# Kernel optimization log

Hardware: AMD Instinct MI355X
Metric: run time of the kernel (lower is better)

The kernel has to match this reference:

```python
import jax, jax.numpy as jnp
import numpy as np

IN_C, H, W = 64, 256, 256
K = 3
OUT_C = 128


def setup_inputs() -> dict:
    key = jax.random.key(0)
    k1, k2 = jax.random.split(key)
    x = jax.random.normal(k1, (IN_C, H, W), dtype=jnp.float32)
    limit = np.sqrt(6.0 / (IN_C * K * K + OUT_C)).astype(np.float32)
    kernels = jax.random.uniform(k2, (OUT_C, IN_C, K, K), minval=-limit, maxval=limit, dtype=jnp.float32)
    biases = jnp.zeros((OUT_C,), dtype=jnp.float32)
    return {"x": x, "kernels": kernels, "biases": biases}


def reference(x, kernels, biases):
    # Cross-correlation (patch * kernel, no flip), VALID padding, CHW single image.
    out = jax.lax.conv_general_dilated(
        x[None],                      # [1, C, H, W]
        kernels,                      # [O, I, K, K]
        window_strides=(1, 1),
        padding="VALID",
        dimension_numbers=("NCHW", "OIHW", "NCHW"),
    )[0]                              # [O, H-K+1, W-K+1]
    return out + biases[:, None, None]
```

## Files before the change

kernel.cpp:

```cpp
#include <hip/hip_runtime.h>
#include <stdint.h>

#define IN_C 64
#define HH 256
#define WW 256
#define HW (HH * WW)
#define OUT_C 128
#define OH 254
#define OW 254
#define OHW (OH * OW)

#define XR 4
#define XW 66
#define CPAD 72

typedef __attribute__((ext_vector_type(4))) float f32x4;
typedef __attribute__((ext_vector_type(8))) __bf16 bf16x8;

__device__ __forceinline__ unsigned short f2bf(float f) {
  union { float f; unsigned u; } v; v.f = f;
  unsigned r = v.u + 0x7FFFu + ((v.u >> 16) & 1u);
  return (unsigned short)(r >> 16);
}

__global__ void prep_w(const float* __restrict__ w, unsigned short* __restrict__ wt) {
  const int idx = blockIdx.x * 256 + threadIdx.x;
  if (idx >= 9 * 8192) return;
  const int j    = idx & 7;
  const int lane = (idx >> 3) & 63;
  const int mt   = (idx >> 9) & 7;
  const int ch   = (idx >> 12) & 1;
  const int tap  = idx >> 13;
  const int o = mt * 16 + (lane & 15);
  const int c = ch * 32 + (lane >> 4) * 8 + j;
  wt[idx] = f2bf(w[(o * IN_C + c) * 9 + tap]);
}

__global__ __launch_bounds__(256, 2) void conv_mfma(
    const float* __restrict__ x, const unsigned short* __restrict__ wt,
    const float* __restrict__ bias, float* __restrict__ out) {
  __shared__ __align__(16) unsigned short Xs[XR * XW * CPAD];

  const int tid  = threadIdx.x;
  const int wave = tid >> 6;
  const int lane = tid & 63;
  const int x0 = blockIdx.x * 64;
  const int y0 = blockIdx.y * 2;

  const int mhalf = wave & 1;
  const int nhalf = wave >> 1;
  const int nlane = lane & 15;
  const int quad  = lane >> 4;

  const bf16x8* __restrict__ Wp = ((const bf16x8*)wt) + lane + (mhalf * 4) * 64;

  bf16x8 afA[4], afB[4];
#pragma unroll
  for (int mt = 0; mt < 4; ++mt) afA[mt] = Wp[mt * 64];

  {
    const int cq = tid & 15;
    const int xh = tid >> 4;
    const float* bx = x + (y0 * WW + x0 + xh * 4);
#pragma unroll
    for (int r = 0; r < XR; ++r) {
      f32x4 vv[4];
#pragma unroll
      for (int cc = 0; cc < 4; ++cc)
        vv[cc] = *(const f32x4*)(bx + (cq * 4 + cc) * HW + r * WW);
#pragma unroll
      for (int xxi = 0; xxi < 4; ++xxi) {
        union { unsigned u[2]; } p;
        p.u[0] = (unsigned)f2bf(vv[0][xxi]) | ((unsigned)f2bf(vv[1][xxi]) << 16);
        p.u[1] = (unsigned)f2bf(vv[2][xxi]) | ((unsigned)f2bf(vv[3][xxi]) << 16);
        *(uint2*)&Xs[(r * XW + xh * 4 + xxi) * CPAD + cq * 4] = make_uint2(p.u[0], p.u[1]);
      }
    }
    if (tid < 128) {
      const int c = tid & 63;
      const int xxt = 64 + (tid >> 6);
      int xg = x0 + xxt;
      if (xg > WW - 1) xg = WW - 1;
#pragma unroll
      for (int r = 0; r < XR; ++r)
        Xs[(r * XW + xxt) * CPAD + c] = f2bf(x[c * HW + (y0 + r) * WW + xg]);
    }
  }

  f32x4 acc[4][4];
#pragma unroll
  for (int mt = 0; mt < 4; ++mt) {
    const f32x4 bv = *(const f32x4*)(bias + (mhalf * 4 + mt) * 16 + quad * 4);
#pragma unroll
    for (int nt = 0; nt < 4; ++nt) acc[mt][nt] = bv;
  }

  __syncthreads();

#pragma unroll 1
  for (int pair = 0; pair < 9; ++pair) {
    const int ky = pair / 3;
    const int kx = pair - ky * 3;
    const int r = nhalf + ky;
    const unsigned short* xrow = &Xs[(r * XW + kx) * CPAD + quad * 8];

#pragma unroll
    for (int mt = 0; mt < 4; ++mt) afB[mt] = Wp[((2 * pair + 1) * 8 + mt) * 64];

    {
      bf16x8 bfr[4];
#pragma unroll
      for (int nt = 0; nt < 4; ++nt)
        bfr[nt] = *(const bf16x8*)&xrow[(nt * 16 + nlane) * CPAD];
#pragma unroll
      for (int mt = 0; mt < 4; ++mt)
#pragma unroll
        for (int nt = 0; nt < 4; ++nt)
          acc[mt][nt] = __builtin_amdgcn_mfma_f32_16x16x32_bf16(afA[mt], bfr[nt], acc[mt][nt], 0, 0, 0);
    }

    if (pair < 8) {
#pragma unroll
      for (int mt = 0; mt < 4; ++mt) afA[mt] = Wp[((2 * pair + 2) * 8 + mt) * 64];
    }

    {
      bf16x8 bfr[4];
#pragma unroll
      for (int nt = 0; nt < 4; ++nt)
        bfr[nt] = *(const bf16x8*)&xrow[(nt * 16 + nlane) * CPAD + 32];
#pragma unroll
      for (int mt = 0; mt < 4; ++mt)
#pragma unroll
        for (int nt = 0; nt < 4; ++nt)
          acc[mt][nt] = __builtin_amdgcn_mfma_f32_16x16x32_bf16(afB[mt], bfr[nt], acc[mt][nt], 0, 0, 0);
    }
  }

  const int y = y0 + nhalf;
#pragma unroll
  for (int mt = 0; mt < 4; ++mt) {
    const int obase = (mhalf * 4 + mt) * 16 + quad * 4;
#pragma unroll
    for (int nt = 0; nt < 4; ++nt) {
      const int xc = x0 + nt * 16 + nlane;
      if (xc < OW) {
        float* dst = out + obase * OHW + y * OW + xc;
#pragma unroll
        for (int reg = 0; reg < 4; ++reg)
          dst[reg * OHW] = acc[mt][nt][reg];
      }
    }
  }
}

extern "C" void kernel_launch(void* const* d_in, const int* in_sizes, int n_in,
                              void* d_out, int out_size, void* d_ws, size_t ws_size,
                              hipStream_t stream) {
  const float* x = (const float*)d_in[0];
  const float* w = (const float*)d_in[1];
  const float* b = (const float*)d_in[2];
  float* out = (float*)d_out;
  unsigned short* wt = (unsigned short*)d_ws;

  prep_w<<<dim3(288), dim3(256), 0, stream>>>(w, wt);
  conv_mfma<<<dim3(4, 127), dim3(256), 0, stream>>>(x, wt, b, out);
}
```

Measured before the change: 89.61 us.

## Pre-convert input to swizzled bf16 HWC layout and stage it via async LDS loads

Adds a prep_x kernel that converts the fp32 CHW input once into a bf16 channel-last layout, storing it in workspace with an XOR swizzle on 16-byte channel chunks. The conv kernel then fills its LDS tile with global_load_lds direct-to-LDS copies, replacing per-block fp32 loads, bf16 conversion and scattered LDS stores. Fragment reads apply the matching XOR swizzle in place of the old padded-row layout to avoid bank conflicts. The cost is an extra launch plus a full read and write pass over the input. The last column block also reads past the row into the next row's or trailing memory; those values feed only outputs that are masked off.

```diff
diff --git a/kernel.cpp b/kernel.cpp
--- a/kernel.cpp
+++ b/kernel.cpp
@@ -10,9 +10,9 @@
 #define OW 254
 #define OHW (OH * OW)
 
-#define XR 4
-#define XW 66
-#define CPAD 72
+#define XB_OFF 262144
+#define XROW 72
+#define XRB (XROW * 128)
 
 typedef __attribute__((ext_vector_type(4))) float f32x4;
 typedef __attribute__((ext_vector_type(8))) __bf16 bf16x8;
@@ -21,6 +21,12 @@
   union { float f; unsigned u; } v; v.f = f;
   unsigned r = v.u + 0x7FFFu + ((v.u >> 16) & 1u);
   return (unsigned short)(r >> 16);
+}
+
+__device__ __forceinline__ void async_lds16(const void* g, void* l) {
+  __builtin_amdgcn_global_load_lds(
+      (const __attribute__((address_space(1))) unsigned int*)g,
+      (__attribute__((address_space(3))) unsigned int*)l, 16, 0, 0);
 }
 
 __global__ void prep_w(const float* __restrict__ w, unsigned short* __restrict__ wt) {
@@ -36,10 +42,37 @@
   wt[idx] = f2bf(w[(o * IN_C + c) * 9 + tap]);
 }
 
+__global__ __launch_bounds__(256) void prep_x(const float* __restrict__ x,
+                                              unsigned short* __restrict__ xb) {
+  const int y = blockIdx.x;
+  const int t = threadIdx.x;
+  const int co = t & 7;
+  const int pg = t >> 3;
+  const float* bx = x + (co * 8) * HW + y * WW + pg * 8;
+  f32x4 v[8][2];
+#pragma unroll
+  for (int cc = 0; cc < 8; ++cc) {
+    v[cc][0] = *(const f32x4*)(bx + cc * HW);
+    v[cc][1] = *(const f32x4*)(bx + cc * HW + 4);
+  }
+#pragma unroll
+  for (int i = 0; i < 8; ++i) {
+    unsigned u[4];
+#pragma unroll
+    for (int p = 0; p < 4; ++p) {
+      const float a = (i < 4) ? v[2 * p][0][i] : v[2 * p][1][i - 4];
+      const float b = (i < 4) ? v[2 * p + 1][0][i] : v[2 * p + 1][1][i - 4];
+      u[p] = (unsigned)f2bf(a) | ((unsigned)f2bf(b) << 16);
+    }
+    const int px = pg * 8 + i;
+    *(uint4*)&xb[(((y * WW + px) * 8) + (co ^ i)) * 8] = make_uint4(u[0], u[1], u[2], u[3]);
+  }
+}
+
 __global__ __launch_bounds__(256, 2) void conv_mfma(
-    const float* __restrict__ x, const unsigned short* __restrict__ wt,
+    const unsigned short* __restrict__ xb, const unsigned short* __restrict__ wt,
     const float* __restrict__ bias, float* __restrict__ out) {
-  __shared__ __align__(16) unsigned short Xs[XR * XW * CPAD];
+  __shared__ __align__(16) char Xs[4 * XRB];
 
   const int tid  = threadIdx.x;
   const int wave = tid >> 6;
@@ -53,37 +86,19 @@
   const int quad  = lane >> 4;
 
   const bf16x8* __restrict__ Wp = ((const bf16x8*)wt) + lane + (mhalf * 4) * 64;
-
   bf16x8 afA[4], afB[4];
 #pragma unroll
   for (int mt = 0; mt < 4; ++mt) afA[mt] = Wp[mt * 64];
 
   {
-    const int cq = tid & 15;
-    const int xh = tid >> 4;
-    const float* bx = x + (y0 * WW + x0 + xh * 4);
+    const char* gb = (const char*)xb;
 #pragma unroll
-    for (int r = 0; r < XR; ++r) {
-      f32x4 vv[4];
-#pragma unroll
-      for (int cc = 0; cc < 4; ++cc)
-        vv[cc] = *(const f32x4*)(bx + (cq * 4 + cc) * HW + r * WW);
-#pragma unroll
-      for (int xxi = 0; xxi < 4; ++xxi) {
-        union { unsigned u[2]; } p;
-        p.u[0] = (unsigned)f2bf(vv[0][xxi]) | ((unsigned)f2bf(vv[1][xxi]) << 16);
-        p.u[1] = (unsigned)f2bf(vv[2][xxi]) | ((unsigned)f2bf(vv[3][xxi]) << 16);
-        *(uint2*)&Xs[(r * XW + xh * 4 + xxi) * CPAD + cq * 4] = make_uint2(p.u[0], p.u[1]);
-      }
-    }
-    if (tid < 128) {
-      const int c = tid & 63;
-      const int xxt = 64 + (tid >> 6);
-      int xg = x0 + xxt;
-      if (xg > WW - 1) xg = WW - 1;
-#pragma unroll
-      for (int r = 0; r < XR; ++r)
-        Xs[(r * XW + xxt) * CPAD + c] = f2bf(x[c * HW + (y0 + r) * WW + xg]);
+    for (int i = 0; i < 9; ++i) {
+      const int c = wave + i * 4;
+      const int r = c / 9;
+      const int k = c - r * 9;
+      async_lds16(gb + (size_t)((y0 + r) * WW + x0) * 128 + k * 1024 + lane * 16,
+                  Xs + r * XRB + k * 1024);
     }
   }
 
@@ -102,7 +117,10 @@
     const int ky = pair / 3;
     const int kx = pair - ky * 3;
     const int r = nhalf + ky;
-    const unsigned short* xrow = &Xs[(r * XW + kx) * CPAD + quad * 8];
+    const int sw = (kx + nlane) & 7;
+    const char* xrow = Xs + r * XRB + (kx + nlane) * 128;
+    const int j0 = (quad ^ sw) * 16;
+    const int j1 = ((4 + quad) ^ sw) * 16;
 
 #pragma unroll
     for (int mt = 0; mt < 4; ++mt) afB[mt] = Wp[((2 * pair + 1) * 8 + mt) * 64];
@@ -111,7 +129,7 @@
       bf16x8 bfr[4];
 #pragma unroll
       for (int nt = 0; nt < 4; ++nt)
-        bfr[nt] = *(const bf16x8*)&xrow[(nt * 16 + nlane) * CPAD];
+        bfr[nt] = *(const bf16x8*)(xrow + nt * 2048 + j0);
 #pragma unroll
       for (int mt = 0; mt < 4; ++mt)
 #pragma unroll
@@ -128,7 +146,7 @@
       bf16x8 bfr[4];
 #pragma unroll
       for (int nt = 0; nt < 4; ++nt)
-        bfr[nt] = *(const bf16x8*)&xrow[(nt * 16 + nlane) * CPAD + 32];
+        bfr[nt] = *(const bf16x8*)(xrow + nt * 2048 + j1);
 #pragma unroll
       for (int mt = 0; mt < 4; ++mt)
 #pragma unroll
@@ -162,7 +180,9 @@
   const float* b = (const float*)d_in[2];
   float* out = (float*)d_out;
   unsigned short* wt = (unsigned short*)d_ws;
+  unsigned short* xb = (unsigned short*)((char*)d_ws + XB_OFF);
 
   prep_w<<<dim3(288), dim3(256), 0, stream>>>(w, wt);
-  conv_mfma<<<dim3(4, 127), dim3(256), 0, stream>>>(x, wt, b, out);
+  prep_x<<<dim3(256), dim3(256), 0, stream>>>(x, xb);
+  conv_mfma<<<dim3(4, 127), dim3(256), 0, stream>>>(xb, wt, b, out);
 }
```

Measured after the change: 94.63 us. 1.06x slower.

## Compute four output rows per block with 512 threads to reuse input halo

Applied to the files above, without the earlier changes.

Each block now loads six input rows into LDS and has eight waves compute four output rows, instead of four input rows feeding two output rows with four waves. This lowers the redundant halo loads and fp32-to-bf16 conversions per output row, and halves the grid. It adds row clamping for the final partial tile and bounds checks on stores. The cost is larger LDS per block and fewer, larger blocks, which may reduce occupancy and load balance across CUs.

```diff
diff --git a/kernel.cpp b/kernel.cpp
--- a/kernel.cpp
+++ b/kernel.cpp
@@ -10,7 +10,7 @@
 #define OW 254
 #define OHW (OH * OW)
 
-#define XR 4
+#define XR 6
 #define XW 66
 #define CPAD 72
 
@@ -36,7 +36,7 @@
   wt[idx] = f2bf(w[(o * IN_C + c) * 9 + tap]);
 }
 
-__global__ __launch_bounds__(256, 2) void conv_mfma(
+__global__ __launch_bounds__(512, 2) void conv_mfma(
     const float* __restrict__ x, const unsigned short* __restrict__ wt,
     const float* __restrict__ bias, float* __restrict__ out) {
   __shared__ __align__(16) unsigned short Xs[XR * XW * CPAD];
@@ -45,45 +45,47 @@
   const int wave = tid >> 6;
   const int lane = tid & 63;
   const int x0 = blockIdx.x * 64;
-  const int y0 = blockIdx.y * 2;
+  const int y0 = blockIdx.y * 4;
 
   const int mhalf = wave & 1;
-  const int nhalf = wave >> 1;
+  const int row   = wave >> 1;
   const int nlane = lane & 15;
   const int quad  = lane >> 4;
 
   const bf16x8* __restrict__ Wp = ((const bf16x8*)wt) + lane + (mhalf * 4) * 64;
-
   bf16x8 afA[4], afB[4];
 #pragma unroll
   for (int mt = 0; mt < 4; ++mt) afA[mt] = Wp[mt * 64];
 
   {
     const int cq = tid & 15;
-    const int xh = tid >> 4;
-    const float* bx = x + (y0 * WW + x0 + xh * 4);
+    const int xh = (tid >> 4) & 15;
+    const int r3 = (tid >> 8) * 3;
 #pragma unroll
-    for (int r = 0; r < XR; ++r) {
+    for (int k = 0; k < 3; ++k) {
+      const int r = r3 + k;
+      const int yr = (y0 + r > 255) ? 255 : (y0 + r);
+      const float* bx = x + yr * WW + x0 + xh * 4;
       f32x4 vv[4];
 #pragma unroll
       for (int cc = 0; cc < 4; ++cc)
-        vv[cc] = *(const f32x4*)(bx + (cq * 4 + cc) * HW + r * WW);
+        vv[cc] = *(const f32x4*)(bx + (cq * 4 + cc) * HW);
 #pragma unroll
       for (int xxi = 0; xxi < 4; ++xxi) {
-        union { unsigned u[2]; } p;
-        p.u[0] = (unsigned)f2bf(vv[0][xxi]) | ((unsigned)f2bf(vv[1][xxi]) << 16);
-        p.u[1] = (unsigned)f2bf(vv[2][xxi]) | ((unsigned)f2bf(vv[3][xxi]) << 16);
-        *(uint2*)&Xs[(r * XW + xh * 4 + xxi) * CPAD + cq * 4] = make_uint2(p.u[0], p.u[1]);
+        unsigned u0 = (unsigned)f2bf(vv[0][xxi]) | ((unsigned)f2bf(vv[1][xxi]) << 16);
+        unsigned u1 = (unsigned)f2bf(vv[2][xxi]) | ((unsigned)f2bf(vv[3][xxi]) << 16);
+        *(uint2*)&Xs[(r * XW + xh * 4 + xxi) * CPAD + cq * 4] = make_uint2(u0, u1);
       }
     }
-    if (tid < 128) {
-      const int c = tid & 63;
-      const int xxt = 64 + (tid >> 6);
+    for (int k = tid; k < 768; k += 512) {
+      const int c = k & 63;
+      const int q = k >> 6;
+      const int xxt = 64 + (q & 1);
+      const int r = q >> 1;
+      const int yr = (y0 + r > 255) ? 255 : (y0 + r);
       int xg = x0 + xxt;
       if (xg > WW - 1) xg = WW - 1;
-#pragma unroll
-      for (int r = 0; r < XR; ++r)
-        Xs[(r * XW + xxt) * CPAD + c] = f2bf(x[c * HW + (y0 + r) * WW + xg]);
+      Xs[(r * XW + xxt) * CPAD + c] = f2bf(x[c * HW + yr * WW + xg]);
     }
   }
 
@@ -101,7 +103,7 @@
   for (int pair = 0; pair < 9; ++pair) {
     const int ky = pair / 3;
     const int kx = pair - ky * 3;
-    const int r = nhalf + ky;
+    const int r = row + ky;
     const unsigned short* xrow = &Xs[(r * XW + kx) * CPAD + quad * 8];
 
 #pragma unroll
@@ -137,18 +139,20 @@
     }
   }
 
-  const int y = y0 + nhalf;
+  const int y = y0 + row;
+  if (y < OH) {
 #pragma unroll
-  for (int mt = 0; mt < 4; ++mt) {
-    const int obase = (mhalf * 4 + mt) * 16 + quad * 4;
+    for (int mt = 0; mt < 4; ++mt) {
+      const int obase = (mhalf * 4 + mt) * 16 + quad * 4;
 #pragma unroll
-    for (int nt = 0; nt < 4; ++nt) {
-      const int xc = x0 + nt * 16 + nlane;
-      if (xc < OW) {
-        float* dst = out + obase * OHW + y * OW + xc;
+      for (int nt = 0; nt < 4; ++nt) {
+        const int xc = x0 + nt * 16 + nlane;
+        if (xc < OW) {
+          float* dst = out + obase * OHW + y * OW + xc;
 #pragma unroll
-        for (int reg = 0; reg < 4; ++reg)
-          dst[reg * OHW] = acc[mt][nt][reg];
+          for (int reg = 0; reg < 4; ++reg)
+            dst[reg * OHW] = acc[mt][nt][reg];
+        }
       }
     }
   }
@@ -164,5 +168,5 @@
   unsigned short* wt = (unsigned short*)d_ws;
 
   prep_w<<<dim3(288), dim3(256), 0, stream>>>(w, wt);
-  conv_mfma<<<dim3(4, 127), dim3(256), 0, stream>>>(x, wt, b, out);
+  conv_mfma<<<dim3(4, 64), dim3(512), 0, stream>>>(x, wt, b, out);
 }
```

New measurement: 88.52 us. Within noise of the previous version (-1.2%).
